# Kernel tuning notes

Measured on AMD Instinct MI355X. Metric: run time of the kernel, lower is better.

The kernel has to match this reference:

```python
import jax, jax.numpy as jnp
import numpy as np

B, M, L = 8, 512, 1024          # batch, block_size, attn_lim (max span)
H, K = 512, 8                   # hidden, heads
D = H // K                      # head_dim = 64
RAMP = 32                       # attn_span_len (soft-mask ramp)
SPAN_INIT = 1.0                 # attn_span_init -> full span, skip_len = 0
SCALE = 1.0 / np.sqrt(D)


def _unskew(X):
    # X: [b, M, M+L] -> [b, M, L]  (relative-position unshift via reshape trick)
    b, m, ml = X.shape
    l = ml - m
    X = X.reshape(b, m * ml)
    X = jnp.pad(X, ((0, 0), (0, m)))
    X = X.reshape(b, m, ml + 1)
    return X[:, :, :l]


def _skew(X):
    # X: [b, M, L] -> [b, M, L+M]  (pad value 0)
    b, m, l = X.shape
    X = jnp.pad(X, ((0, 0), (0, 0), (0, m + 1)))
    X = X.reshape(b, -1)[:, : m * (l + m)]
    return X.reshape(b, m, l + m)


def _heads(x):
    # [B, S, H] -> [B*K, S, D]
    b, s, _ = x.shape
    return x.reshape(b, s, K, D).transpose(0, 2, 1, 3).reshape(b * K, s, D)


def setup_inputs() -> dict:
    key0 = jax.random.key(0)
    ks = jax.random.split(key0, 8)
    s = 0.02
    return {
        "query": jax.random.normal(ks[0], (B, M, H), jnp.float32),
        "key": jax.random.normal(ks[1], (B, M + L, H), jnp.float32),
        "value": jax.random.normal(ks[2], (B, M + L, H), jnp.float32),
        "key_pe": jax.random.normal(ks[3], (1, D, L), jnp.float32) * s,
        "Wq": jax.random.normal(ks[4], (H, H), jnp.float32) * s,
        "Wk": jax.random.normal(ks[5], (H, H), jnp.float32) * s,
        "Wv": jax.random.normal(ks[6], (H, H), jnp.float32) * s,
        "Wo": jax.random.normal(ks[7], (H, H), jnp.float32) * s,
        "span_val": jnp.full((K, 1, 1), SPAN_INIT, jnp.float32),
    }


def reference(query, key, value, key_pe, Wq, Wk, Wv, Wo, span_val):
    # QKV projections (nn.Linear, no bias: y = x @ W.T) + head split
    q = _heads(query @ Wq.T)     # [B*K, M, D]
    k = _heads(key @ Wk.T)       # [B*K, M+L, D]
    v = _heads(value @ Wv.T)     # [B*K, M+L, D]

    # content attention + unskew to relative coordinates
    attn_cont = _unskew(jnp.einsum('bmd,bnd->bmn', q, k))    # [B*K, M, L]
    # positional attention (shared across batch/heads via key_pe[1,D,L])
    attn_pos = jnp.einsum('bmd,dl->bml', q, key_pe[0])       # [B*K, M, L]

    attn = jax.nn.softmax((attn_cont + attn_pos) * SCALE, axis=-1)

    # adaptive span soft mask, per head (skip_len = 0)
    template = jnp.linspace(1.0 - L, 0.0, L, dtype=jnp.float32)        # [L]
    mask = jnp.clip((template + span_val * L) / RAMP + 1.0, 0.0, 1.0)  # [K,1,L]
    attn = (attn.reshape(B, K, M, L) * mask[None]).reshape(B * K, M, L)

    # skew back to absolute coords and contract with values
    out = jnp.matmul(_skew(attn), v)                         # [B*K, M, D]
    out = out.reshape(B, K, M, D).transpose(0, 2, 1, 3).reshape(B, M, H)
    return out @ Wo.T
```

## Files before the change

### kernel.cpp

```cpp
#include <hip/hip_runtime.h>
#include <hip/hip_bf16.h>
#include <type_traits>

typedef __hip_bfloat16 bf16;
typedef short bf16x8 __attribute__((ext_vector_type(8)));
typedef float f32x4 __attribute__((ext_vector_type(4)));
typedef short short4_ __attribute__((ext_vector_type(4)));

#define NB 8
#define SM 512
#define SL 1024
#define SH 512
#define NH 8
#define HD 64
#define SN 1536

static __device__ __forceinline__ short bf_bits(float x) {
  union { bf16 b; short s; } u; u.b = __float2bfloat16(x); return u.s;
}
static __device__ __forceinline__ bf16x8 ld8any(const bf16* p) {
  return *reinterpret_cast<const bf16x8*>(p);
}
static __device__ __forceinline__ bf16x8 ld8any(const float* p) {
  float4 a = *reinterpret_cast<const float4*>(p);
  float4 b = *reinterpret_cast<const float4*>(p + 4);
  bf16x8 r;
  r[0] = bf_bits(a.x); r[1] = bf_bits(a.y); r[2] = bf_bits(a.z); r[3] = bf_bits(a.w);
  r[4] = bf_bits(b.x); r[5] = bf_bits(b.y); r[6] = bf_bits(b.z); r[7] = bf_bits(b.w);
  return r;
}
static __device__ __forceinline__ void st1(bf16* p, float v) { *p = __float2bfloat16(v); }
static __device__ __forceinline__ void st1(float* p, float v) { *p = v; }
static __device__ __forceinline__ f32x4 mfma16(bf16x8 a, bf16x8 b, f32x4 c) {
  return __builtin_amdgcn_mfma_f32_16x16x32_bf16(a, b, c, 0, 0, 0);
}

static __device__ __forceinline__ void frag_store8(const float* __restrict__ src,
                                                   bf16* __restrict__ dst, int i) {
  const size_t flat = (size_t)i * 8;
  const int row = (int)(flat >> 9), k = (int)(flat & 511);
  const size_t a = (size_t)(row >> 4) * 8192 + (size_t)(k >> 5) * 512
                 + (size_t)(((k >> 3) & 3) * 128 + (row & 15) * 8);
  *reinterpret_cast<bf16x8*>(dst + a) = ld8any(src + flat);
}

__global__ __launch_bounds__(256) void prep_all(
    const float* __restrict__ key, const float* __restrict__ value,
    const float* __restrict__ query,
    const float* __restrict__ Wq, const float* __restrict__ Wk,
    const float* __restrict__ Wv, const float* __restrict__ Wo,
    const float* __restrict__ pe,
    bf16* __restrict__ kS, bf16* __restrict__ vS, bf16* __restrict__ qS,
    bf16* __restrict__ Wb, bf16* __restrict__ peF) {
  const int id = blockIdx.x, tid = threadIdx.x;
  if (id < 3072) {
    frag_store8(key, kS, id * 256 + tid);
  } else if (id < 6144) {
    frag_store8(value, vS, (id - 3072) * 256 + tid);
  } else if (id < 7168) {
    frag_store8(query, qS, (id - 6144) * 256 + tid);
  } else if (id < 7680) {
    const int s = id - 7168;
    const float* srcs[4] = {Wq, Wk, Wv, Wo};
    frag_store8(srcs[s >> 7], Wb + (size_t)(s >> 7) * 262144,
                (s & 127) * 256 + tid);
  } else {
    const int idx = (id - 7680) * 256 + tid;
    const int l = idx >> 6, d = idx & 63;
    peF[(size_t)((l>>4)*2 + (d>>5))*512
        + (size_t)((((d>>3)&3)*16 + (l&15))*8 + (d&7))]
      = __float2bfloat16(pe[d * SL + l]);
  }
}

#define T2STR 136

#define GLOADF(AF, BF, KT)                                                   \
  {                                                                          \
    AF[0] = ld8any(xr +         (size_t)(KT) * 512);                         \
    AF[1] = ld8any(xr + 8192  + (size_t)(KT) * 512);                         \
    AF[2] = ld8any(xr + 16384 + (size_t)(KT) * 512);                         \
    AF[3] = ld8any(xr + 24576 + (size_t)(KT) * 512);                         \
    BF[0] = ld8any(wr +         (size_t)(KT) * 512);                         \
    BF[1] = ld8any(wr + 8192  + (size_t)(KT) * 512);                         \
  }

template <int MODE, typename TY>
static __device__ __forceinline__ void gemm_dev(const bf16* __restrict__ XF,
                                                const bf16* __restrict__ WF,
                                                TY* __restrict__ Y,
                                                int id, bf16* tile) {
  const int s_   = id >> 3;
  const int xblk = (id & 7) + 8 * (s_ >> 3);
  const int yblk = s_ & 7;
  const int tid  = threadIdx.x;
  const int lane = tid & 63, w = tid >> 6;
  const int col16 = lane & 15, quad = lane >> 4;
  const int lane8 = lane * 8;
  const int wm = w >> 1, wn = w & 1;
  const int m0 = xblk * 128 + wm * 64;
  const int n0 = yblk * 64 + wn * 32;
  const bf16* xr = XF + (size_t)(m0 >> 4) * 8192 + lane8;
  const bf16* wr = WF + (size_t)(n0 >> 4) * 8192 + lane8;
  f32x4 acc[4][2];
#pragma unroll
  for (int i = 0; i < 4; ++i)
#pragma unroll
    for (int j = 0; j < 2; ++j) acc[i][j] = f32x4{0.f,0.f,0.f,0.f};

  bf16x8 afA[4], bfA[2], afB[4], bfB[2];
  GLOADF(afA, bfA, 0);
  __builtin_amdgcn_sched_barrier(0);
#pragma unroll
  for (int kt = 0; kt < 16; kt += 2) {
    GLOADF(afB, bfB, kt + 1);
    __builtin_amdgcn_sched_barrier(0);
#pragma unroll
    for (int mt = 0; mt < 4; ++mt)
#pragma unroll
      for (int nt = 0; nt < 2; ++nt)
        acc[mt][nt] = mfma16(afA[mt], bfA[nt], acc[mt][nt]);
    const int ktn = (kt + 2 < 16) ? kt + 2 : kt;
    GLOADF(afA, bfA, ktn);
    __builtin_amdgcn_sched_barrier(0);
#pragma unroll
    for (int mt = 0; mt < 4; ++mt)
#pragma unroll
      for (int nt = 0; nt < 2; ++nt)
        acc[mt][nt] = mfma16(afB[mt], bfB[nt], acc[mt][nt]);
  }

  if constexpr (MODE == 0) {
#pragma unroll
    for (int mt = 0; mt < 4; ++mt)
#pragma unroll
      for (int r = 0; r < 4; ++r) {
        const int row = m0 + mt*16 + quad*4 + r;
        TY* yr = Y + (size_t)row * SH + n0 + col16;
        st1(yr,      acc[mt][0][r]);
        st1(yr + 16, acc[mt][1][r]);
      }
  } else if constexpr (MODE == 1) {
    const int dq = col16 >> 3, de = col16 & 7;
#pragma unroll
    for (int mt = 0; mt < 4; ++mt)
#pragma unroll
      for (int r = 0; r < 4; ++r) {
        const int row = m0 + mt*16 + quad*4 + r;
        const int b = row / SN, sr = row - b * SN;
        bf16* yr = (bf16*)Y
            + ((((size_t)(b*NH + yblk)*96 + (sr>>4))*2 + wn)*512)
            + (size_t)((sr&15)*8 + dq*128 + de);
        yr[0]   = __float2bfloat16(acc[mt][0][r]);
        yr[256] = __float2bfloat16(acc[mt][1][r]);
      }
  } else if constexpr (MODE == 3) {
    const int dq2 = col16 >> 3, de = col16 & 7;
#pragma unroll
    for (int mt = 0; mt < 4; ++mt)
#pragma unroll
      for (int r = 0; r < 4; ++r) {
        bf16* yr = (bf16*)Y + (size_t)((m0>>4) + mt) * 8192
                 + (size_t)(yblk*2 + wn) * 512
                 + (size_t)(dq2*128 + (quad*4 + r)*8 + de);
        yr[0]   = __float2bfloat16(acc[mt][0][r]);
        yr[256] = __float2bfloat16(acc[mt][1][r]);
      }
  } else {
#pragma unroll
    for (int mt = 0; mt < 4; ++mt)
#pragma unroll
      for (int r = 0; r < 4; ++r) {
        const int row_loc = wm*64 + mt*16 + quad*4 + r;
#pragma unroll
        for (int nt = 0; nt < 2; ++nt) {
          const int d = wn*32 + nt*16 + col16;
          tile[d * T2STR + row_loc] = __float2bfloat16(acc[mt][nt][r]);
        }
      }
    __syncthreads();
    const int d  = tid >> 2;
    const int hq = tid & 3;
    const bf16* src = tile + d * T2STR + hq * 32;
    const int row0 = xblk*128 + hq*32;
    const int b = row0 / SN, sr0 = row0 - b * SN;
    const int hb2 = b*NH + yblk;
    bf16* dstF = (bf16*)Y + (((size_t)hb2*4 + (d>>4))*96)*256 + (size_t)(d&15)*8;
#pragma unroll
    for (int i = 0; i < 4; ++i) {
      const int key = sr0 + i*8;
      const size_t off = (size_t)(key>>4)*256 + (size_t)((key>>3)&1)*128;
      *reinterpret_cast<uint4*>(dstF + off) = reinterpret_cast<const uint4*>(src)[i];
    }
  }
}

__global__ __launch_bounds__(256) void gemmKQ(
    const bf16* __restrict__ XK, const bf16* __restrict__ WK, bf16* __restrict__ YK,
    const bf16* __restrict__ XQ, const bf16* __restrict__ WQ, bf16* __restrict__ YQ) {
  __shared__ bf16 dummy[8];
  const int id = blockIdx.x;
  if (id < 768) gemm_dev<1, bf16>(XK, WK, YK, id, dummy);
  else          gemm_dev<3, bf16>(XQ, WQ, YQ, id - 768, dummy);
}

__global__ __launch_bounds__(256) void gemmV(
    const bf16* __restrict__ XF, const bf16* __restrict__ WF, bf16* __restrict__ Y) {
  __shared__ __align__(16) bf16 tile[64 * T2STR];
  gemm_dev<2, bf16>(XF, WF, Y, blockIdx.x, tile);
}

__global__ __launch_bounds__(256) void gemmO(
    const bf16* __restrict__ XF, const bf16* __restrict__ WF, float* __restrict__ Y) {
  __shared__ bf16 dummy[8];
  gemm_dev<0, float>(XF, WF, Y, blockIdx.x, dummy);
}

#define PSTR1 69
#define BSTR1 104

__global__ __launch_bounds__(64, 2) void attn1w(
    const bf16* __restrict__ qp, const bf16* __restrict__ Kh,
    const bf16* __restrict__ VT, const bf16* __restrict__ peT,
    const float* __restrict__ spanv, bf16* __restrict__ ctx) {
  __shared__ __align__(16) float pos_s[16 * PSTR1];
  __shared__ __align__(16) bf16  P_s[16 * BSTR1];

  const int id = blockIdx.x;
  const int h  = id & 7;
  const int s_ = id >> 3;
  const int m0 = (s_ & 31) * 16;
  const int b  = s_ >> 5;
  const int hb = b * 8 + h;
  const int lane  = threadIdx.x;
  const int col16 = lane & 15, quad = lane >> 4, kq = quad << 3;
  const int q4 = quad << 2;
  const int lane8 = lane * 8;

  for (int i = lane; i < 16 * BSTR1; i += 64)
    P_s[i] = __float2bfloat16(0.0f);

  const bf16* qb = qp + (size_t)((b*SM + m0) >> 4) * 8192 + h*1024 + lane8;
  const bf16x8 qf0 = ld8any(qb), qf1 = ld8any(qb + 512);

  const bf16* kbF = Kh + (size_t)hb * 98304 + lane8;
  const bf16* vbF = VT + (size_t)hb * 98304 + lane8;
  const bf16* pbF = peT + lane8;

  float Mrun = -1.0e30f, Srun = 0.0f;
  const float span1024 = spanv[h] * 1024.0f;
  f32x4 o[4];
#pragma unroll
  for (int dt = 0; dt < 4; ++dt) o[dt] = f32x4{0.f,0.f,0.f,0.f};

  bf16x8 kf[5][2], pf[4][2], vf[4][3];

  {
    const int tk0 = m0 >> 4;
#pragma unroll
    for (int t = 0; t < 5; ++t) {
      const bf16* kr = kbF + (size_t)(tk0 + t) * 1024;
      kf[t][0] = ld8any(kr); kf[t][1] = ld8any(kr + 512);
    }
#pragma unroll
    for (int t = 0; t < 4; ++t) {
      const bf16* pr = pbF + (size_t)t * 1024;
      pf[t][0] = ld8any(pr); pf[t][1] = ld8any(pr + 512);
    }
#pragma unroll
    for (int dt = 0; dt < 4; ++dt) {
      const bf16* v0 = vbF + (size_t)dt * 24576 + (size_t)tk0 * 256;
#pragma unroll
      for (int ks = 0; ks < 3; ++ks) vf[dt][ks] = ld8any(v0 + ks*512);
    }
    __builtin_amdgcn_sched_barrier(0);
  }

  const int posw = col16 * PSTR1 + q4;
  const int posr = col16 * (PSTR1 - 1) + q4;
  const int pww  = col16 * BSTR1 + q4;
  const int pwr  = col16 * BSTR1 + kq;

  for (int ch = 0; ch < 16; ++ch) {
    const int l0 = ch << 6;

    f32x4 pacc[4];
#pragma unroll
    for (int t = 0; t < 4; ++t) {
      f32x4 a = {0.f,0.f,0.f,0.f};
      a = mfma16(pf[t][0], qf0, a);
      a = mfma16(pf[t][1], qf1, a);
      pacc[t] = a;
    }
#pragma unroll
    for (int t = 0; t < 4; ++t)
#pragma unroll
      for (int r = 0; r < 4; ++r)
        pos_s[posw + 16*t + r] = pacc[t][r];

    f32x4 cacc[5];
#pragma unroll
    for (int t = 0; t < 5; ++t) {
      f32x4 a = {0.f,0.f,0.f,0.f};
      a = mfma16(kf[t][0], qf0, a);
      a = mfma16(kf[t][1], qf1, a);
      cacc[t] = a;
    }

    {
      const int l0n = (ch < 15) ? l0 + 64 : l0;
      const int tkn = (m0 + l0n) >> 4;
      const int tpn = l0n >> 4;
#pragma unroll
      for (int t = 0; t < 5; ++t) {
        const bf16* kr = kbF + (size_t)(tkn + t) * 1024;
        kf[t][0] = ld8any(kr); kf[t][1] = ld8any(kr + 512);
      }
#pragma unroll
      for (int t = 0; t < 4; ++t) {
        const bf16* pr = pbF + (size_t)(tpn + t) * 1024;
        pf[t][0] = ld8any(pr); pf[t][1] = ld8any(pr + 512);
      }
      __builtin_amdgcn_sched_barrier(0);
    }

    float sc[5][4];
    float mc = -1.0e30f;
#pragma unroll
    for (int t = 0; t < 5; ++t) {
      const f32x4 pv4 = *reinterpret_cast<const f32x4*>(&pos_s[posr + 16*t]);
#pragma unroll
      for (int r = 0; r < 4; ++r) {
        const int l = 16*t + q4 + r - col16;
        float v = (cacc[t][r] + pv4[r]) * 0.125f;
        v = ((unsigned)l < 64u) ? v : -1.0e30f;
        sc[t][r] = v;
        mc = fmaxf(mc, v);
      }
    }
    mc = fmaxf(mc, __shfl_xor(mc, 16));
    mc = fmaxf(mc, __shfl_xor(mc, 32));
    const float Mnew = fmaxf(Mrun, mc);
    const float alpha = __expf(Mrun - Mnew);
    float ls = 0.0f;
#pragma unroll
    for (int t = 0; t < 5; ++t) {
      short4_ pk;
#pragma unroll
      for (int r = 0; r < 4; ++r) {
        const float p = __expf(sc[t][r] - Mnew);
        ls += p;
        const float lg = (float)(l0 + 16*t + q4 + r - col16);
        float mv = (lg - 1023.0f + span1024) * 0.03125f + 1.0f;
        mv = fminf(fmaxf(mv, 0.0f), 1.0f);
        pk[r] = bf_bits(p * mv);
      }
      *reinterpret_cast<short4_*>(&P_s[pww + 16*t]) = pk;
    }
    ls += __shfl_xor(ls, 16);
    ls += __shfl_xor(ls, 32);
    Srun = Srun * alpha + ls;
    Mrun = Mnew;

#pragma unroll
    for (int dt = 0; dt < 4; ++dt)
#pragma unroll
      for (int r = 0; r < 4; ++r) o[dt][r] *= alpha;
#pragma unroll
    for (int ks = 0; ks < 3; ++ks) {
      const bf16x8 ap = ld8any(&P_s[pwr + ks*32]);
#pragma unroll
      for (int dt = 0; dt < 4; ++dt)
        o[dt] = mfma16(vf[dt][ks], ap, o[dt]);
    }

    {
      const int tkn = (m0 + ((ch < 15) ? l0 + 64 : l0)) >> 4;
#pragma unroll
      for (int dt = 0; dt < 4; ++dt) {
        const bf16* v0 = vbF + (size_t)dt * 24576 + (size_t)tkn * 256;
#pragma unroll
        for (int ks = 0; ks < 3; ++ks) vf[dt][ks] = ld8any(v0 + ks*512);
      }
      __builtin_amdgcn_sched_barrier(0);
    }
  }

  const float inv = 1.0f / Srun;
  bf16* crb = ctx + (size_t)((b*SM + m0) >> 4) * 8192
            + (size_t)(h*1024 + (quad>>1)*128 + col16*8 + (quad&1)*4);
#pragma unroll
  for (int dt = 0; dt < 4; ++dt) {
    short4_ pk;
#pragma unroll
    for (int r = 0; r < 4; ++r) pk[r] = bf_bits(o[dt][r] * inv);
    *reinterpret_cast<short4_*>(crb + (size_t)(dt>>1)*512 + (dt&1)*256) = pk;
  }
}

template <int MODE, typename TX, typename TW, typename TY>
__global__ __launch_bounds__(256) void gemmbn64(const TX* __restrict__ X,
                                                const TW* __restrict__ W,
                                                TY* __restrict__ Y) {
  __shared__ __align__(16) bf16 tile[(MODE == 2) ? 64 * T2STR : 8];
  const int id   = blockIdx.x;
  const int s_   = id >> 3;
  const int xblk = (id & 7) + 8 * (s_ >> 3);
  const int yblk = s_ & 7;
  const int tid  = threadIdx.x;
  const int lane = tid & 63, w = tid >> 6;
  const int col16 = lane & 15, quad = lane >> 4, kq = quad << 3;
  const int wm = w >> 1, wn = w & 1;
  const int m0 = xblk * 128 + wm * 64;
  const int n0 = yblk * 64 + wn * 32;
  const TX* xr = X + (size_t)(m0 + col16) * SH + kq;
  const TW* wr = W + (size_t)(n0 + col16) * SH + kq;
  f32x4 acc[4][2];
#pragma unroll
  for (int i = 0; i < 4; ++i)
#pragma unroll
    for (int j = 0; j < 2; ++j) acc[i][j] = f32x4{0.f,0.f,0.f,0.f};
#pragma unroll
  for (int k0 = 0; k0 < SH; k0 += 32) {
    bf16x8 af[4], bfr[2];
#pragma unroll
    for (int t = 0; t < 4; ++t) af[t]  = ld8any(xr + (size_t)(t*16) * SH + k0);
#pragma unroll
    for (int t = 0; t < 2; ++t) bfr[t] = ld8any(wr + (size_t)(t*16) * SH + k0);
#pragma unroll
    for (int mt = 0; mt < 4; ++mt)
#pragma unroll
      for (int nt = 0; nt < 2; ++nt)
        acc[mt][nt] = mfma16(af[mt], bfr[nt], acc[mt][nt]);
  }

  if constexpr (MODE == 0) {
#pragma unroll
    for (int mt = 0; mt < 4; ++mt)
#pragma unroll
      for (int r = 0; r < 4; ++r) {
        const int row = m0 + mt*16 + quad*4 + r;
        TY* yr = Y + (size_t)row * SH + n0 + col16;
        st1(yr,      acc[mt][0][r]);
        st1(yr + 16, acc[mt][1][r]);
      }
  } else if constexpr (MODE == 1) {
#pragma unroll
    for (int mt = 0; mt < 4; ++mt)
#pragma unroll
      for (int r = 0; r < 4; ++r) {
        const int row = m0 + mt*16 + quad*4 + r;
        const int b = row / SN, sr = row - b * SN;
        bf16* yr = (bf16*)Y + (size_t)((b*NH + yblk)*SN + sr) * HD
                 + wn*32 + col16;
        yr[0]  = __float2bfloat16(acc[mt][0][r]);
        yr[16] = __float2bfloat16(acc[mt][1][r]);
      }
  } else {
#pragma unroll
    for (int mt = 0; mt < 4; ++mt)
#pragma unroll
      for (int r = 0; r < 4; ++r) {
        const int row_loc = wm*64 + mt*16 + quad*4 + r;
#pragma unroll
        for (int nt = 0; nt < 2; ++nt) {
          const int d = wn*32 + nt*16 + col16;
          tile[d * T2STR + row_loc] = __float2bfloat16(acc[mt][nt][r]);
        }
      }
    __syncthreads();
    const int d  = tid >> 2;
    const int hq = tid & 3;
    const bf16* src = tile + d * T2STR + hq * 32;
    const int row0 = xblk*128 + hq*32;
    const int b = row0 / SN, sr0 = row0 - b * SN;
    bf16* dst = (bf16*)Y + (size_t)((b*NH + yblk)*HD + d) * SN + sr0;
#pragma unroll
    for (int i = 0; i < 4; ++i)
      reinterpret_cast<uint4*>(dst)[i] = reinterpret_cast<const uint4*>(src)[i];
  }
}

__global__ void transpose_pe_fb(const float* __restrict__ pe, bf16* __restrict__ peT) {
  int idx = blockIdx.x * 256 + threadIdx.x;
  int l = idx >> 6, d = idx & 63;
  peT[idx] = __float2bfloat16(pe[d * SL + l]);
}

#define MT 16
#define CSTR 84
#define PSTR 65
#define BSTR 104
#define QSTR 72

__global__ __launch_bounds__(128) void attn_kernel_fb(
    const float* __restrict__ query, const float* __restrict__ Wq,
    const bf16* __restrict__ Kh, const bf16* __restrict__ VT,
    const bf16* __restrict__ peT, const float* __restrict__ spanv,
    bf16* __restrict__ ctx) {
  __shared__ __align__(16) float cont_lds[MT][CSTR];
  __shared__ __align__(16) float pos_lds[MT][PSTR];
  __shared__ __align__(16) bf16  P_lds[MT][BSTR];
  __shared__ __align__(16) bf16  q_lds[MT*QSTR];
  __shared__ float alpha_lds[MT];
  __shared__ float S_lds[MT];

  const int id = blockIdx.x;
  const int h  = id & 7;
  const int s_ = id >> 3;
  const int m0 = (s_ & 31) * MT;
  const int b  = s_ >> 5;
  const int hb = b * 8 + h;
  const int tid  = threadIdx.x;
  const int lane = tid & 63;
  const int w    = tid >> 6;
  const int col16 = lane & 15, quad = lane >> 4, kq = quad << 3;
  const int wr = quad << 2;

  for (int i = tid; i < MT * BSTR; i += 128)
    (&P_lds[0][0])[i] = __float2bfloat16(0.0f);

  bf16x8 qf0, qf1;
  {
    f32x4 qa0 = {0.f,0.f,0.f,0.f}, qa1 = qa0;
    const float* xq = query + (size_t)(b*SM + m0 + col16) * SH + kq;
    const float* w0 = Wq + (size_t)(h*HD + w*32 + col16) * SH + kq;
    const float* w1 = w0 + (size_t)16 * SH;
#pragma unroll
    for (int k0 = 0; k0 < SH; k0 += 32) {
      bf16x8 xa = ld8any(xq + k0);
      qa0 = mfma16(xa, ld8any(w0 + k0), qa0);
      qa1 = mfma16(xa, ld8any(w1 + k0), qa1);
    }
#pragma unroll
    for (int r = 0; r < 4; ++r) {
      q_lds[(wr + r)*QSTR + w*32 + col16]      = __float2bfloat16(qa0[r]);
      q_lds[(wr + r)*QSTR + w*32 + 16 + col16] = __float2bfloat16(qa1[r]);
    }
    __syncthreads();
    qf0 = ld8any(&q_lds[col16*QSTR + kq]);
    qf1 = ld8any(&q_lds[col16*QSTR + kq + 32]);
  }

  const bf16* kb = Kh + (size_t)(hb * SN) * HD + kq;
  const bf16* vb = VT + (size_t)(hb * HD) * SN;

  const int srow = tid >> 3, sj = tid & 7;
  float Mrun = -1.0e30f, Srun = 0.0f;
  const float span = spanv[h];
  const int dt0 = w * 16, dt1 = (w + 2) * 16;
  f32x4 o0 = {0.f,0.f,0.f,0.f}, o1 = o0;

  for (int ch = 0; ch < 16; ++ch) {
    const int l0 = ch << 6;
    const int nb_ = m0 + l0;

    f32x4 ca0 = {0.f,0.f,0.f,0.f}, ca1 = ca0, ca2 = ca0, pa0 = ca0, pa1 = ca0;
    {
      const bf16* kr0 = kb + (size_t)(nb_ + w*16 + col16) * HD;
      ca0 = mfma16(qf0, ld8any(kr0),           ca0);
      ca0 = mfma16(qf1, ld8any(kr0 + 32),      ca0);
      const bf16* kr1 = kr0 + 32 * HD;
      ca1 = mfma16(qf0, ld8any(kr1),           ca1);
      ca1 = mfma16(qf1, ld8any(kr1 + 32),      ca1);
      if (w == 0) {
        const bf16* kr2 = kr0 + 64 * HD;
        ca2 = mfma16(qf0, ld8any(kr2),         ca2);
        ca2 = mfma16(qf1, ld8any(kr2 + 32),    ca2);
      }
      const bf16* pr0 = peT + (size_t)(l0 + w*16 + col16) * HD + kq;
      pa0 = mfma16(qf0, ld8any(pr0),           pa0);
      pa0 = mfma16(qf1, ld8any(pr0 + 32),      pa0);
      const bf16* pr1 = pr0 + 32 * HD;
      pa1 = mfma16(qf0, ld8any(pr1),           pa1);
      pa1 = mfma16(qf1, ld8any(pr1 + 32),      pa1);
    }
#pragma unroll
    for (int r = 0; r < 4; ++r) {
      cont_lds[wr + r][w*16 + col16]      = ca0[r];
      cont_lds[wr + r][w*16 + 32 + col16] = ca1[r];
      if (w == 0) cont_lds[wr + r][64 + col16] = ca2[r];
      pos_lds[wr + r][w*16 + col16]       = pa0[r];
      pos_lds[wr + r][w*16 + 32 + col16]  = pa1[r];
    }
    __syncthreads();

    float sc[8];
    float mc = -1.0e30f;
    const float* crow = &cont_lds[srow][srow + sj*8];
    const float* prow = &pos_lds[srow][sj*8];
#pragma unroll
    for (int i = 0; i < 8; ++i) {
      float v = (crow[i] + prow[i]) * 0.125f;
      sc[i] = v;
      mc = fmaxf(mc, v);
    }
    mc = fmaxf(mc, __shfl_xor(mc, 1));
    mc = fmaxf(mc, __shfl_xor(mc, 2));
    mc = fmaxf(mc, __shfl_xor(mc, 4));
    const float Mnew = fmaxf(Mrun, mc);
    const float alpha = __expf(Mrun - Mnew);
    float ls = 0.0f;
    bf16* pwrow = &P_lds[srow][srow + sj*8];
#pragma unroll
    for (int i = 0; i < 8; ++i) {
      float p = __expf(sc[i] - Mnew);
      ls += p;
      const float tpl = (float)(l0 + sj*8 + i) - 1023.0f;
      float mv = (tpl + span * 1024.0f) * 0.03125f + 1.0f;
      mv = fminf(fmaxf(mv, 0.0f), 1.0f);
      pwrow[i] = __float2bfloat16(p * mv);
    }
    ls += __shfl_xor(ls, 1);
    ls += __shfl_xor(ls, 2);
    ls += __shfl_xor(ls, 4);
    Srun = Srun * alpha + ls;
    Mrun = Mnew;
    if (sj == 0) { alpha_lds[srow] = alpha; S_lds[srow] = Srun; }
    __syncthreads();

    float al[4];
#pragma unroll
    for (int r = 0; r < 4; ++r) al[r] = alpha_lds[wr + r];
#pragma unroll
    for (int r = 0; r < 4; ++r) { o0[r] *= al[r]; o1[r] *= al[r]; }
#pragma unroll
    for (int ks = 0; ks < 3; ++ks) {
      const bf16x8 ap = ld8any(&P_lds[col16][ks*32 + kq]);
      const bf16* v0 = vb + (size_t)(dt0 + col16) * SN + nb_ + ks*32 + kq;
      const bf16* v1 = vb + (size_t)(dt1 + col16) * SN + nb_ + ks*32 + kq;
      o0 = mfma16(ap, ld8any(v0), o0);
      o1 = mfma16(ap, ld8any(v1), o1);
    }
  }

  bf16* cr = ctx + (size_t)(b*SM + m0 + wr) * SH + h*HD + col16;
#pragma unroll
  for (int r = 0; r < 4; ++r) {
    const float inv = 1.0f / S_lds[wr + r];
    cr[(size_t)r * SH + dt0] = __float2bfloat16(o0[r] * inv);
    cr[(size_t)r * SH + dt1] = __float2bfloat16(o1[r] * inv);
  }
}

extern "C" void kernel_launch(void* const* d_in, const int* in_sizes, int n_in,
                              void* d_out, int out_size, void* d_ws, size_t ws_size,
                              hipStream_t stream) {
  const float* query  = (const float*)d_in[0];
  const float* key    = (const float*)d_in[1];
  const float* value  = (const float*)d_in[2];
  const float* key_pe = (const float*)d_in[3];
  const float* Wq     = (const float*)d_in[4];
  const float* Wk     = (const float*)d_in[5];
  const float* Wv     = (const float*)d_in[6];
  const float* Wo     = (const float*)d_in[7];
  const float* spanv  = (const float*)d_in[8];
  float* out = (float*)d_out;

  bf16* ws = (bf16*)d_ws;
  if (ws_size >= (size_t)48365568) {
    bf16* B0   = ws;
    bf16* B1   = B0  + 6291456;
    bf16* B2   = B1  + 6291456;
    bf16* qp   = B2  + 6291456;
    bf16* ctxC = qp  + 2097152;
    bf16* peF  = ctxC + 2097152;
    bf16* Wb   = peF + 65536;
    bf16* Wq_b = Wb, *Wk_b = Wb + 262144, *Wv_b = Wb + 524288, *Wo_b = Wb + 786432;

    prep_all<<<7936, 256, 0, stream>>>(key, value, query, Wq, Wk, Wv, Wo,
                                       key_pe, B0, B1, ctxC, Wb, peF);
    gemmKQ<<<1024, 256, 0, stream>>>(B0, Wk_b, B2, ctxC, Wq_b, qp);
    gemmV<<<768, 256, 0, stream>>>(B1, Wv_b, B0);
    attn1w<<<2048, 64, 0, stream>>>(qp, B2, B0, peF, spanv, ctxC);
    gemmO<<<256, 256, 0, stream>>>(ctxC, Wo_b, out);
  } else {
    bf16* k_head = ws;
    bf16* vT     = k_head + 6291456;
    bf16* ctx    = vT     + 6291456;
    bf16* peT    = ctx    + 2097152;
    gemmbn64<1, float, float, bf16><<<768, 256, 0, stream>>>(key,   Wk, k_head);
    gemmbn64<2, float, float, bf16><<<768, 256, 0, stream>>>(value, Wv, vT);
    transpose_pe_fb<<<256, 256, 0, stream>>>(key_pe, peT);
    attn_kernel_fb<<<2048, 128, 0, stream>>>(query, Wq, k_head, vT,
                                             peT, spanv, ctx);
    gemmbn64<0, bf16, float, float><<<256, 256, 0, stream>>>(ctx, Wo, out);
  }
}
```

Measured before the change: 190.4 us.

## Double GEMM N-tile to 128 and stage prep fragment layout through LDS

The projection GEMMs now compute 128x128 output tiles per block instead of 128x64. Each wave holds a 4x4 accumulator grid, so the A-fragment loads are reused across twice as many MFMAs, and the grids for the K/Q, V and O GEMMs are halved. The prep kernel now converts whole 16-row slabs: it writes row-major bf16 into LDS, then emits the fragment-ordered layout with contiguous global stores instead of scattered ones. The costs are higher register pressure, fewer blocks (only 128 for gemmO, which may underfill the CUs), and a larger LDS tile.

```diff
diff --git a/kernel.cpp b/kernel.cpp
--- a/kernel.cpp
+++ b/kernel.cpp
@@ -35,14 +35,6 @@
   return __builtin_amdgcn_mfma_f32_16x16x32_bf16(a, b, c, 0, 0, 0);
 }
 
-static __device__ __forceinline__ void frag_store8(const float* __restrict__ src,
-                                                   bf16* __restrict__ dst, int i) {
-  const size_t flat = (size_t)i * 8;
-  const int row = (int)(flat >> 9), k = (int)(flat & 511);
-  const size_t a = (size_t)(row >> 4) * 8192 + (size_t)(k >> 5) * 512
-                 + (size_t)(((k >> 3) & 3) * 128 + (row & 15) * 8);
-  *reinterpret_cast<bf16x8*>(dst + a) = ld8any(src + flat);
-}
 
 __global__ __launch_bounds__(256) void prep_all(
     const float* __restrict__ key, const float* __restrict__ value,
@@ -52,30 +44,49 @@
     const float* __restrict__ pe,
     bf16* __restrict__ kS, bf16* __restrict__ vS, bf16* __restrict__ qS,
     bf16* __restrict__ Wb, bf16* __restrict__ peF) {
+  __shared__ __align__(16) bf16 t[16 * 520];
   const int id = blockIdx.x, tid = threadIdx.x;
-  if (id < 3072) {
-    frag_store8(key, kS, id * 256 + tid);
-  } else if (id < 6144) {
-    frag_store8(value, vS, (id - 3072) * 256 + tid);
-  } else if (id < 7168) {
-    frag_store8(query, qS, (id - 6144) * 256 + tid);
-  } else if (id < 7680) {
-    const int s = id - 7168;
-    const float* srcs[4] = {Wq, Wk, Wv, Wo};
-    frag_store8(srcs[s >> 7], Wb + (size_t)(s >> 7) * 262144,
-                (s & 127) * 256 + tid);
+  if (id < 1920) {
+    const float* src; bf16* dst;
+    if (id < 768)       { src = key   + (size_t)id * 8192;
+                          dst = kS    + (size_t)id * 8192; }
+    else if (id < 1536) { src = value + (size_t)(id - 768) * 8192;
+                          dst = vS    + (size_t)(id - 768) * 8192; }
+    else if (id < 1792) { src = query + (size_t)(id - 1536) * 8192;
+                          dst = qS    + (size_t)(id - 1536) * 8192; }
+    else {
+      const int s = id - 1792;
+      const float* ws_[4] = {Wq, Wk, Wv, Wo};
+      src = ws_[s >> 5] + (size_t)(s & 31) * 8192;
+      dst = Wb + (size_t)(s >> 5) * 262144 + (size_t)(s & 31) * 8192;
+    }
+#pragma unroll
+    for (int j = 0; j < 4; ++j) {
+      const int i = j * 2048 + tid * 8;
+      const bf16x8 v = ld8any(src + i);
+      *reinterpret_cast<bf16x8*>(&t[(i >> 9) * 520 + (i & 511)]) = v;
+    }
+    __syncthreads();
+#pragma unroll
+    for (int j = 0; j < 4; ++j) {
+      const int a = j * 2048 + tid * 8;
+      const int kt5 = a >> 9, rest = a & 511;
+      const int q = rest >> 7, rowl = (rest >> 3) & 15;
+      *reinterpret_cast<bf16x8*>(dst + a) =
+          *reinterpret_cast<const bf16x8*>(&t[rowl * 520 + kt5 * 32 + q * 8]);
+    }
   } else {
-    const int idx = (id - 7680) * 256 + tid;
+    const int idx = (id - 1920) * 256 + tid;
     const int l = idx >> 6, d = idx & 63;
-    peF[(size_t)((l>>4)*2 + (d>>5))*512
-        + (size_t)((((d>>3)&3)*16 + (l&15))*8 + (d&7))]
+    peF[(size_t)((l >> 4) * 2 + (d >> 5)) * 512
+        + (size_t)((((d >> 3) & 3) * 16 + (l & 15)) * 8 + (d & 7))]
       = __float2bfloat16(pe[d * SL + l]);
   }
 }
 
 #define T2STR 136
 
-#define GLOADF(AF, BF, KT)                                                   \
+#define GL2(AF, BF, KT)                                                      \
   {                                                                          \
     AF[0] = ld8any(xr +         (size_t)(KT) * 512);                         \
     AF[1] = ld8any(xr + 8192  + (size_t)(KT) * 512);                         \
@@ -83,50 +94,50 @@
     AF[3] = ld8any(xr + 24576 + (size_t)(KT) * 512);                         \
     BF[0] = ld8any(wr +         (size_t)(KT) * 512);                         \
     BF[1] = ld8any(wr + 8192  + (size_t)(KT) * 512);                         \
+    BF[2] = ld8any(wr + 16384 + (size_t)(KT) * 512);                         \
+    BF[3] = ld8any(wr + 24576 + (size_t)(KT) * 512);                         \
   }
 
 template <int MODE, typename TY>
-static __device__ __forceinline__ void gemm_dev(const bf16* __restrict__ XF,
-                                                const bf16* __restrict__ WF,
-                                                TY* __restrict__ Y,
-                                                int id, bf16* tile) {
-  const int s_   = id >> 3;
-  const int xblk = (id & 7) + 8 * (s_ >> 3);
-  const int yblk = s_ & 7;
+static __device__ __forceinline__ void gemm_dev2(const bf16* __restrict__ XF,
+                                                 const bf16* __restrict__ WF,
+                                                 TY* __restrict__ Y,
+                                                 int id, bf16* tile) {
+  const int yblk = id & 3, xblk = id >> 2;
   const int tid  = threadIdx.x;
   const int lane = tid & 63, w = tid >> 6;
   const int col16 = lane & 15, quad = lane >> 4;
   const int lane8 = lane * 8;
   const int wm = w >> 1, wn = w & 1;
   const int m0 = xblk * 128 + wm * 64;
-  const int n0 = yblk * 64 + wn * 32;
+  const int n0 = yblk * 128 + wn * 64;
   const bf16* xr = XF + (size_t)(m0 >> 4) * 8192 + lane8;
   const bf16* wr = WF + (size_t)(n0 >> 4) * 8192 + lane8;
-  f32x4 acc[4][2];
+  f32x4 acc[4][4];
 #pragma unroll
   for (int i = 0; i < 4; ++i)
 #pragma unroll
-    for (int j = 0; j < 2; ++j) acc[i][j] = f32x4{0.f,0.f,0.f,0.f};
-
-  bf16x8 afA[4], bfA[2], afB[4], bfB[2];
-  GLOADF(afA, bfA, 0);
+    for (int j = 0; j < 4; ++j) acc[i][j] = f32x4{0.f,0.f,0.f,0.f};
+
+  bf16x8 afA[4], bfA[4], afB[4], bfB[4];
+  GL2(afA, bfA, 0);
   __builtin_amdgcn_sched_barrier(0);
 #pragma unroll
   for (int kt = 0; kt < 16; kt += 2) {
-    GLOADF(afB, bfB, kt + 1);
+    GL2(afB, bfB, kt + 1);
     __builtin_amdgcn_sched_barrier(0);
 #pragma unroll
     for (int mt = 0; mt < 4; ++mt)
 #pragma unroll
-      for (int nt = 0; nt < 2; ++nt)
+      for (int nt = 0; nt < 4; ++nt)
         acc[mt][nt] = mfma16(afA[mt], bfA[nt], acc[mt][nt]);
     const int ktn = (kt + 2 < 16) ? kt + 2 : kt;
-    GLOADF(afA, bfA, ktn);
+    GL2(afA, bfA, ktn);
     __builtin_amdgcn_sched_barrier(0);
 #pragma unroll
     for (int mt = 0; mt < 4; ++mt)
 #pragma unroll
-      for (int nt = 0; nt < 2; ++nt)
+      for (int nt = 0; nt < 4; ++nt)
         acc[mt][nt] = mfma16(afB[mt], bfB[nt], acc[mt][nt]);
   }
 
@@ -137,11 +148,12 @@
       for (int r = 0; r < 4; ++r) {
         const int row = m0 + mt*16 + quad*4 + r;
         TY* yr = Y + (size_t)row * SH + n0 + col16;
-        st1(yr,      acc[mt][0][r]);
-        st1(yr + 16, acc[mt][1][r]);
+#pragma unroll
+        for (int nt = 0; nt < 4; ++nt) st1(yr + nt*16, acc[mt][nt][r]);
       }
   } else if constexpr (MODE == 1) {
     const int dq = col16 >> 3, de = col16 & 7;
+    const int head = n0 >> 6;
 #pragma unroll
     for (int mt = 0; mt < 4; ++mt)
 #pragma unroll
@@ -149,22 +161,24 @@
         const int row = m0 + mt*16 + quad*4 + r;
         const int b = row / SN, sr = row - b * SN;
         bf16* yr = (bf16*)Y
-            + ((((size_t)(b*NH + yblk)*96 + (sr>>4))*2 + wn)*512)
-            + (size_t)((sr&15)*8 + dq*128 + de);
-        yr[0]   = __float2bfloat16(acc[mt][0][r]);
-        yr[256] = __float2bfloat16(acc[mt][1][r]);
+            + (((size_t)(b*NH + head)*96 + (sr>>4))*2)*512
+            + (size_t)((sr&15)*8 + de);
+#pragma unroll
+        for (int nt = 0; nt < 4; ++nt)
+          yr[(nt>>1)*512 + ((nt&1)*2 + dq)*128] = __float2bfloat16(acc[mt][nt][r]);
       }
   } else if constexpr (MODE == 3) {
-    const int dq2 = col16 >> 3, de = col16 & 7;
+    const int dq = col16 >> 3, de = col16 & 7;
+    const int c5b = n0 >> 5;
 #pragma unroll
     for (int mt = 0; mt < 4; ++mt)
 #pragma unroll
       for (int r = 0; r < 4; ++r) {
         bf16* yr = (bf16*)Y + (size_t)((m0>>4) + mt) * 8192
-                 + (size_t)(yblk*2 + wn) * 512
-                 + (size_t)(dq2*128 + (quad*4 + r)*8 + de);
-        yr[0]   = __float2bfloat16(acc[mt][0][r]);
-        yr[256] = __float2bfloat16(acc[mt][1][r]);
+                 + (size_t)((quad*4 + r)*8 + de);
+#pragma unroll
+        for (int nt = 0; nt < 4; ++nt)
+          yr[(c5b + (nt>>1))*512 + ((nt&1)*2 + dq)*128] = __float2bfloat16(acc[mt][nt][r]);
       }
   } else {
 #pragma unroll
@@ -173,21 +187,23 @@
       for (int r = 0; r < 4; ++r) {
         const int row_loc = wm*64 + mt*16 + quad*4 + r;
 #pragma unroll
-        for (int nt = 0; nt < 2; ++nt) {
-          const int d = wn*32 + nt*16 + col16;
+        for (int nt = 0; nt < 4; ++nt) {
+          const int d = wn*64 + nt*16 + col16;
           tile[d * T2STR + row_loc] = __float2bfloat16(acc[mt][nt][r]);
         }
       }
     __syncthreads();
-    const int d  = tid >> 2;
-    const int hq = tid & 3;
-    const bf16* src = tile + d * T2STR + hq * 32;
-    const int row0 = xblk*128 + hq*32;
+    const int d  = tid >> 1;
+    const int hq = tid & 1;
+    const bf16* src = tile + d * T2STR + hq * 64;
+    const int row0 = xblk*128 + hq*64;
     const int b = row0 / SN, sr0 = row0 - b * SN;
-    const int hb2 = b*NH + yblk;
-    bf16* dstF = (bf16*)Y + (((size_t)hb2*4 + (d>>4))*96)*256 + (size_t)(d&15)*8;
-#pragma unroll
-    for (int i = 0; i < 4; ++i) {
+    const int head = yblk*2 + (d >> 6);
+    const int dd = d & 63;
+    bf16* dstF = (bf16*)Y + (((size_t)(b*NH + head)*4 + (dd>>4))*96)*256
+               + (size_t)(dd&15)*8;
+#pragma unroll
+    for (int i = 0; i < 8; ++i) {
       const int key = sr0 + i*8;
       const size_t off = (size_t)(key>>4)*256 + (size_t)((key>>3)&1)*128;
       *reinterpret_cast<uint4*>(dstF + off) = reinterpret_cast<const uint4*>(src)[i];
@@ -195,25 +211,25 @@
   }
 }
 
-__global__ __launch_bounds__(256) void gemmKQ(
+__global__ __launch_bounds__(256, 2) void gemmKQ(
     const bf16* __restrict__ XK, const bf16* __restrict__ WK, bf16* __restrict__ YK,
     const bf16* __restrict__ XQ, const bf16* __restrict__ WQ, bf16* __restrict__ YQ) {
   __shared__ bf16 dummy[8];
   const int id = blockIdx.x;
-  if (id < 768) gemm_dev<1, bf16>(XK, WK, YK, id, dummy);
-  else          gemm_dev<3, bf16>(XQ, WQ, YQ, id - 768, dummy);
-}
-
-__global__ __launch_bounds__(256) void gemmV(
+  if (id < 384) gemm_dev2<1, bf16>(XK, WK, YK, id, dummy);
+  else          gemm_dev2<3, bf16>(XQ, WQ, YQ, id - 384, dummy);
+}
+
+__global__ __launch_bounds__(256, 2) void gemmV(
     const bf16* __restrict__ XF, const bf16* __restrict__ WF, bf16* __restrict__ Y) {
-  __shared__ __align__(16) bf16 tile[64 * T2STR];
-  gemm_dev<2, bf16>(XF, WF, Y, blockIdx.x, tile);
-}
-
-__global__ __launch_bounds__(256) void gemmO(
+  __shared__ __align__(16) bf16 tile[128 * T2STR];
+  gemm_dev2<2, bf16>(XF, WF, Y, blockIdx.x, tile);
+}
+
+__global__ __launch_bounds__(256, 2) void gemmO(
     const bf16* __restrict__ XF, const bf16* __restrict__ WF, float* __restrict__ Y) {
   __shared__ bf16 dummy[8];
-  gemm_dev<0, float>(XF, WF, Y, blockIdx.x, dummy);
+  gemm_dev2<0, float>(XF, WF, Y, blockIdx.x, dummy);
 }
 
 #define PSTR1 69
@@ -668,12 +684,12 @@
     bf16* Wb   = peF + 65536;
     bf16* Wq_b = Wb, *Wk_b = Wb + 262144, *Wv_b = Wb + 524288, *Wo_b = Wb + 786432;
 
-    prep_all<<<7936, 256, 0, stream>>>(key, value, query, Wq, Wk, Wv, Wo,
+    prep_all<<<1952, 256, 0, stream>>>(key, value, query, Wq, Wk, Wv, Wo,
                                        key_pe, B0, B1, ctxC, Wb, peF);
-    gemmKQ<<<1024, 256, 0, stream>>>(B0, Wk_b, B2, ctxC, Wq_b, qp);
-    gemmV<<<768, 256, 0, stream>>>(B1, Wv_b, B0);
+    gemmKQ<<<512, 256, 0, stream>>>(B0, Wk_b, B2, ctxC, Wq_b, qp);
+    gemmV<<<384, 256, 0, stream>>>(B1, Wv_b, B0);
     attn1w<<<2048, 64, 0, stream>>>(qp, B2, B0, peF, spanv, ctxC);
-    gemmO<<<256, 256, 0, stream>>>(ctxC, Wo_b, out);
+    gemmO<<<128, 256, 0, stream>>>(ctxC, Wo_b, out);
   } else {
     bf16* k_head = ws;
     bf16* vT     = k_head + 6291456;
```

After: 186.2 us. 2.2% less time.
